# Optimization experiments

Measured on AMD Instinct MI355X. Metric: run time of the kernel, lower is better.

The kernel has to match this reference:

```python
import jax, jax.numpy as jnp
import numpy as np

N = 100000   # nodes
P = 3        # metapaths
E = 800000   # edges per metapath (avg degree 8)
IN = 128     # in_size
H = 4        # layer_num_heads
D = 32       # out_size per head
HID = 64     # semantic attention hidden
NEG_SLOPE = 0.2


def setup_inputs() -> dict:
    key = jax.random.key(0)
    ks = jax.random.split(key, 10)
    h = jax.random.normal(ks[0], (N, IN), jnp.float32)
    edge_src = jax.random.randint(ks[1], (P, E), 0, N, dtype=jnp.int32).astype(jnp.int64)
    edge_dst = jax.random.randint(ks[2], (P, E), 0, N, dtype=jnp.int32).astype(jnp.int64)
    W = jax.random.normal(ks[3], (P, IN, H * D), jnp.float32) * 0.05
    attn_l = jax.random.normal(ks[4], (P, H, D), jnp.float32) * 0.05
    attn_r = jax.random.normal(ks[5], (P, H, D), jnp.float32) * 0.05
    bias = jnp.zeros((P, H * D), jnp.float32)
    sa_w1 = jax.random.normal(ks[6], (H * D, HID), jnp.float32) * 0.05
    sa_b1 = jnp.zeros((HID,), jnp.float32)
    sa_w2 = jax.random.normal(ks[7], (HID, 1), jnp.float32) * 0.05
    return {"h": h, "edge_src": edge_src, "edge_dst": edge_dst, "W": W,
            "attn_l": attn_l, "attn_r": attn_r, "bias": bias,
            "sa_w1": sa_w1, "sa_b1": sa_b1, "sa_w2": sa_w2}


def _gat_conv(h, src, dst, Wp, al, ar, bp):
    # DGL GATConv: project, per-edge additive attention, edge softmax over dst, scatter-sum.
    n = h.shape[0]
    feat = (h @ Wp).reshape(n, H, D)              # [N,H,D]
    el = (feat * al).sum(-1)                      # [N,H]
    er = (feat * ar).sum(-1)                      # [N,H]
    e = jax.nn.leaky_relu(el[src] + er[dst], NEG_SLOPE)   # [E,H]
    emax = jax.ops.segment_max(e, dst, num_segments=n)    # [N,H]
    emax = jnp.where(jnp.isfinite(emax), emax, 0.0)       # zero-in-degree guard
    ex = jnp.exp(e - emax[dst])                            # [E,H]
    denom = jax.ops.segment_sum(ex, dst, num_segments=n)   # [N,H]
    alpha = ex / jnp.maximum(denom[dst], 1e-9)              # [E,H]
    msg = alpha[:, :, None] * feat[src]                     # [E,H,D]
    out = jax.ops.segment_sum(msg, dst, num_segments=n)     # [N,H,D]
    return out.reshape(n, H * D) + bp


def reference(h, edge_src, edge_dst, W, attn_l, attn_r, bias, sa_w1, sa_b1, sa_w2):
    embs = []
    for p in range(P):  # small fixed metapath set
        embs.append(_gat_conv(h, edge_src[p], edge_dst[p], W[p], attn_l[p], attn_r[p], bias[p]))
    z = jnp.stack(embs, axis=1)                 # [N,P,H*D]
    # SemanticAttention: MLP score, mean over nodes, softmax over metapaths
    w = (jnp.tanh(z @ sa_w1 + sa_b1) @ sa_w2).mean(0)   # [P,1]
    beta = jax.nn.softmax(w, axis=0)                     # [P,1]
    return (beta[None, :, :] * z).sum(1)                 # [N,H*D]
```

## Files before the change

kernel.cpp:

```cpp
#include <hip/hip_runtime.h>
#include <hip/hip_bf16.h>
#include <math.h>

#define NN 100000
#define NP 3
#define NE 800000
#define NH 4
#define ND 32
#define HD 128
#define NHID 64

#define SLW 256
#define SBK 512
#define GB 391
#define NBLK 196
#define ECHUNK 4096
#define EPT 16
#define EMAX 2368

typedef __attribute__((ext_vector_type(8))) short short8;
typedef __attribute__((ext_vector_type(4))) float f32x4;

__device__ __forceinline__ unsigned short f2bf(float f) {
  union { float f; unsigned int u; } v; v.f = f;
  unsigned int r = v.u + 0x7FFFu + ((v.u >> 16) & 1u);
  return (unsigned short)(r >> 16);
}
__device__ __forceinline__ float bf2f(unsigned short u) {
  return __uint_as_float(((unsigned int)u) << 16);
}
__device__ __forceinline__ float tanh_fast(float x) {
  return 1.f - 2.f / (1.f + __expf(2.f * x));
}

__global__ __launch_bounds__(256) void prep_fill_kernel(
    const float* __restrict__ h, const float* __restrict__ W, const float* __restrict__ W1,
    const int* __restrict__ src_all, const int* __restrict__ dst_all,
    unsigned short* __restrict__ hb, unsigned short* __restrict__ WT,
    unsigned short* __restrict__ W1T, float* __restrict__ s,
    int* __restrict__ cntA, int* __restrict__ baseA, int* __restrict__ pairs) {
  __shared__ int hist[SBK];
  __shared__ int scanb[SBK];
  const int tid = threadIdx.x;
  const int bx = blockIdx.x;
  if (bx < 12500) {
    int i = bx * 256 + tid;
    if (i < NN * 32) {
      float4 v = ((const float4*)h)[i];
      ushort4 o;
      o.x = f2bf(v.x); o.y = f2bf(v.y); o.z = f2bf(v.z); o.w = f2bf(v.w);
      ((ushort4*)hb)[i] = o;
    }
    if (i < NP * 128 * 128) {
      int p = i >> 14, r = i & 16383, n = r >> 7, k = r & 127;
      WT[i] = f2bf(W[(size_t)p * 16384 + k * 128 + n]);
    }
    if (i < NHID * 128) {
      int n = i >> 7, k = i & 127;
      W1T[i] = f2bf(W1[(size_t)k * NHID + n]);
    }
    if (i < 4) s[i] = 0.f;
    return;
  }
  const int b2 = bx - 12500;
  const int p = b2 / NBLK, blk = b2 % NBLK;
  const int* dstp = dst_all + (size_t)p * NE;
  const int* srcp = src_all + (size_t)p * NE;
  hist[tid] = 0; hist[tid + 256] = 0;
  __syncthreads();
  int dv[EPT], sv[EPT];
#pragma unroll
  for (int k = 0; k < EPT; ++k) {
    int e = blk * ECHUNK + k * 256 + tid;
    dv[k] = -1; sv[k] = 0;
    if (e < NE) {
      dv[k] = __builtin_nontemporal_load(dstp + e);
      sv[k] = __builtin_nontemporal_load(srcp + e);
    }
    if (dv[k] >= 0) atomicAdd(&hist[(unsigned)dv[k] >> 8], 1);
  }
  __syncthreads();
  scanb[tid] = hist[tid]; scanb[tid + 256] = hist[tid + 256];
  __syncthreads();
  for (int off = 1; off < SBK; off <<= 1) {
    int a0 = (tid >= off) ? scanb[tid - off] : 0;
    int a1 = scanb[tid + 256 - off];
    __syncthreads();
    scanb[tid] += a0; scanb[tid + 256] += a1;
    __syncthreads();
  }
  int c0 = hist[tid], c1 = hist[tid + 256];
  int b0 = scanb[tid] - c0, b1 = scanb[tid + 256] - c1;
  int* cA = cntA + ((size_t)p * NBLK + blk) * SBK;
  int* bA = baseA + ((size_t)p * NBLK + blk) * SBK;
  cA[tid] = c0; cA[tid + 256] = c1;
  bA[tid] = b0; bA[tid + 256] = b1;
  __syncthreads();
  scanb[tid] = b0; scanb[tid + 256] = b1;
  hist[tid] = 0; hist[tid + 256] = 0;
  __syncthreads();
  int* prp = pairs + (size_t)p * NE + (size_t)blk * ECHUNK;
#pragma unroll
  for (int k = 0; k < EPT; ++k) {
    if (dv[k] >= 0) {
      int sl = (unsigned)dv[k] >> 8;
      int pos = scanb[sl] + atomicAdd(&hist[sl], 1);
      prp[pos] = ((dv[k] & 255) << 17) | sv[k];
    }
  }
}

__global__ __launch_bounds__(256) void gemm_mfma_kernel(
    const unsigned short* __restrict__ hb, const unsigned short* __restrict__ WT_all,
    const float* __restrict__ al_all, const float* __restrict__ ar_all,
    unsigned short* __restrict__ featb_all, float* __restrict__ el_all,
    float* __restrict__ er_all) {
  __shared__ unsigned short Bs[128 * 128];
  const int p = blockIdx.y;
  const unsigned short* WTp = WT_all + (size_t)p * 16384;
#pragma unroll
  for (int it = 0; it < 8; ++it)
    ((float4*)Bs)[it * 256 + threadIdx.x] = ((const float4*)WTp)[it * 256 + threadIdx.x];
  __syncthreads();

  const int wid = threadIdx.x >> 6, lane = threadIdx.x & 63;
  const int c = lane & 15, q = lane >> 4;
  const int tile = blockIdx.x * 4 + wid;
  const int tc = tile < 6250 ? tile : 6249;

  f32x4 acc[8];
#pragma unroll
  for (int t = 0; t < 8; ++t) acc[t] = (f32x4){0.f, 0.f, 0.f, 0.f};

  const unsigned short* arow = hb + (size_t)(tc * 16 + c) * 128 + q * 8;
#pragma unroll
  for (int kc = 0; kc < 4; ++kc) {
    short8 a = *(const short8*)(arow + kc * 32);
#pragma unroll
    for (int t = 0; t < 8; ++t) {
      short8 b = *(const short8*)(Bs + (size_t)(t * 16 + c) * 128 + kc * 32 + q * 8);
      acc[t] = __builtin_amdgcn_mfma_f32_16x16x32_bf16(a, b, acc[t], 0, 0, 0);
    }
  }
  if (tile >= 6250) return;

  unsigned short* featb = featb_all + (size_t)p * NN * 128;
#pragma unroll
  for (int t = 0; t < 8; ++t)
#pragma unroll
    for (int i = 0; i < 4; ++i)
      featb[(size_t)(tc * 16 + q * 4 + i) * 128 + t * 16 + c] = f2bf(acc[t][i]);

  const float* al = al_all + p * 128;
  const float* ar = ar_all + p * 128;
  float alv[8], arv[8];
#pragma unroll
  for (int t = 0; t < 8; ++t) { alv[t] = al[t * 16 + c]; arv[t] = ar[t * 16 + c]; }
  float elp[4][4], erp[4][4];
#pragma unroll
  for (int i = 0; i < 4; ++i)
#pragma unroll
    for (int hh = 0; hh < 4; ++hh) {
      elp[i][hh] = acc[2 * hh][i] * alv[2 * hh] + acc[2 * hh + 1][i] * alv[2 * hh + 1];
      erp[i][hh] = acc[2 * hh][i] * arv[2 * hh] + acc[2 * hh + 1][i] * arv[2 * hh + 1];
    }
#pragma unroll
  for (int m = 1; m <= 8; m <<= 1)
#pragma unroll
    for (int i = 0; i < 4; ++i)
#pragma unroll
      for (int hh = 0; hh < 4; ++hh) {
        elp[i][hh] += __shfl_xor(elp[i][hh], m);
        erp[i][hh] += __shfl_xor(erp[i][hh], m);
      }
  if (c == 0) {
    float* el = el_all + (size_t)p * NN * 4;
    float* er = er_all + (size_t)p * NN * 4;
#pragma unroll
    for (int i = 0; i < 4; ++i) {
      int row = tc * 16 + q * 4 + i;
      *(float4*)(el + (size_t)row * 4) = make_float4(elp[i][0], elp[i][1], elp[i][2], elp[i][3]);
      *(float4*)(er + (size_t)row * 4) = make_float4(erp[i][0], erp[i][1], erp[i][2], erp[i][3]);
    }
  }
}

__global__ __launch_bounds__(512) void fillB2a_kernel(
    const int* __restrict__ cntA, const int* __restrict__ baseA,
    const int* __restrict__ pairs, int* __restrict__ srtpk,
    int2* __restrict__ rowidx, int* __restrict__ btot) {
  __shared__ int scnt[NBLK];
  __shared__ int sbase[NBLK];
  __shared__ int scum[NBLK];
  __shared__ int totE;
  __shared__ int hist[SLW];
  __shared__ int start[SLW];
  __shared__ int wcur[SLW];
  __shared__ int earr[EMAX];
  const int tid = threadIdx.x;
  const int p = blockIdx.y, sl = blockIdx.x;
  const size_t base = ((size_t)p * GB + sl) * EMAX;

  for (int b = tid; b < NBLK; b += 512) {
    scnt[b] = cntA[((size_t)p * NBLK + b) * SBK + sl];
    sbase[b] = baseA[((size_t)p * NBLK + b) * SBK + sl];
  }
  if (tid < SLW) hist[tid] = 0;
  __syncthreads();
  if (tid < NBLK) scum[tid] = scnt[tid];
  __syncthreads();
  for (int off = 1; off < NBLK; off <<= 1) {
    int a = (tid < NBLK && tid >= off) ? scum[tid - off] : 0;
    __syncthreads();
    if (tid < NBLK) scum[tid] += a;
    __syncthreads();
  }
  if (tid == NBLK - 1) { int t = scum[NBLK - 1]; totE = t > EMAX ? EMAX : t; }
  int excl = (tid < NBLK) ? scum[tid] - scnt[tid] : 0;
  __syncthreads();
  if (tid < NBLK) scum[tid] = excl;
  __syncthreads();
  const int total = totE;
  const int* prp = pairs + (size_t)p * NE;
  for (int e = tid; e < total; e += 512) {
    int lo = 0, hi = NBLK - 1;
    while (lo < hi) { int mid = (lo + hi + 1) >> 1; if (scum[mid] <= e) lo = mid; else hi = mid - 1; }
    int pk = prp[(size_t)lo * ECHUNK + sbase[lo] + (e - scum[lo])];
    earr[e] = pk;
    atomicAdd(&hist[pk >> 17], 1);
  }
  __syncthreads();
  if (tid < SLW) start[tid] = hist[tid];
  __syncthreads();
  for (int off = 1; off < SLW; off <<= 1) {
    int a = (tid < SLW && tid >= off) ? start[tid - off] : 0;
    __syncthreads();
    if (tid < SLW) start[tid] += a;
    __syncthreads();
  }
  if (tid < SLW) { int st = start[tid] - hist[tid]; start[tid] = st; wcur[tid] = st; }
  __syncthreads();
  for (int e = tid; e < total; e += 512) {
    int pk = earr[e];
    int pos = atomicAdd(&wcur[pk >> 17], 1);
    srtpk[base + pos] = pk;
  }
  if (tid < SLW) {
    int n = sl * SLW + tid;
    if (n < NN) rowidx[(size_t)p * NN + n] = make_int2((int)(base + start[tid]), hist[tid]);
  }
  if (tid == 0) btot[p * GB + sl] = total;
}

__global__ __launch_bounds__(256) void fillB2b_kernel(
    const int* __restrict__ srtpk, const int* __restrict__ btot,
    const float* __restrict__ el_all, const float* __restrict__ er_all,
    float4* __restrict__ xs) {
  const int p = blockIdx.y, sl = blockIdx.x;
  const int total = btot[p * GB + sl];
  const size_t base = ((size_t)p * GB + sl) * EMAX;
  const float* el = el_all + (size_t)p * NN * 4;
  const float* er = er_all + (size_t)p * NN * 4;
  for (int i = threadIdx.x; i < total; i += 256) {
    int pk = srtpk[base + i];
    int src = pk & 0x1FFFF, dl = pk >> 17;
    int n = sl * SLW + dl;
    float4 ev = *(const float4*)(el + (size_t)src * 4);
    float4 rv = *(const float4*)(er + (size_t)n * 4);
    float4 x;
    float e0 = ev.x + rv.x; e0 = fmaxf(e0, 0.2f * e0); x.x = __expf(e0);
    float e1 = ev.y + rv.y; e1 = fmaxf(e1, 0.2f * e1); x.y = __expf(e1);
    float e2 = ev.z + rv.z; e2 = fmaxf(e2, 0.2f * e2); x.z = __expf(e2);
    float e3 = ev.w + rv.w; e3 = fmaxf(e3, 0.2f * e3); x.w = __expf(e3);
    xs[base + i] = x;
  }
}

__global__ __launch_bounds__(256) void gather4_kernel(
    const unsigned short* __restrict__ featb_all, const int* __restrict__ srtpk,
    const float* __restrict__ xs, const int2* __restrict__ rowidx,
    const float* __restrict__ bias_all, unsigned short* __restrict__ zb) {
  const int p = blockIdx.y;
  const unsigned short* featb = featb_all + (size_t)p * NN * 128;
  const int q = threadIdx.x >> 4;
  const int c16 = threadIdx.x & 15;
  const int hh = c16 >> 2;
  const int n = blockIdx.x * 16 + q;
  int2 rd = rowidx[(size_t)p * NN + n];
  const int rbase = rd.x, deg = rd.y;

  float acc[8] = {0.f, 0.f, 0.f, 0.f, 0.f, 0.f, 0.f, 0.f};
  float dsum = 0.f;

  for (int j = 0; j < deg; j += 4) {
#pragma unroll
    for (int u = 0; u < 4; ++u) {
      int jj = j + u;
      bool v = jj < deg;
      int idx = rbase + jj;
      int pk = v ? srtpk[idx] : 0;
      float x = v ? xs[(size_t)idx * 4 + hh] : 0.f;
      int s = pk & 0x1FFFF;
      short8 f = *(const short8*)(featb + (size_t)s * 128 + c16 * 8);
      dsum += x;
#pragma unroll
      for (int k = 0; k < 8; ++k) acc[k] += x * bf2f((unsigned short)f[k]);
    }
  }

  float rdn = dsum > 0.f ? 1.f / dsum : 0.f;
  const float* bias = bias_all + p * 128 + c16 * 8;
  float4 b0 = *(const float4*)(bias);
  float4 b1 = *(const float4*)(bias + 4);
  short8 o;
  o[0] = f2bf(acc[0] * rdn + b0.x); o[1] = f2bf(acc[1] * rdn + b0.y);
  o[2] = f2bf(acc[2] * rdn + b0.z); o[3] = f2bf(acc[3] * rdn + b0.w);
  o[4] = f2bf(acc[4] * rdn + b1.x); o[5] = f2bf(acc[5] * rdn + b1.y);
  o[6] = f2bf(acc[6] * rdn + b1.z); o[7] = f2bf(acc[7] * rdn + b1.w);
  *(short8*)(zb + (size_t)n * (NP * 128) + p * 128 + c16 * 8) = o;
}

__global__ __launch_bounds__(256) void sem_mfma_kernel(
    const unsigned short* __restrict__ zb, const unsigned short* __restrict__ W1T,
    const float* __restrict__ b1, const float* __restrict__ w2,
    float* __restrict__ s) {
  __shared__ float red3[3];
  if (threadIdx.x < 3) red3[threadIdx.x] = 0.f;
  __syncthreads();
  const int wid = threadIdx.x >> 6, lane = threadIdx.x & 63;
  const int tile = blockIdx.x * 4 + wid;
  const bool active = tile < 18750;
  const int tc = active ? tile : 18749;
  const int c = lane & 15, q = lane >> 4;
  f32x4 acc[4];
#pragma unroll
  for (int t = 0; t < 4; ++t) acc[t] = (f32x4){0.f, 0.f, 0.f, 0.f};

  const unsigned short* arow = zb + (size_t)(tc * 16 + c) * 128 + q * 8;
  const unsigned short* brow = W1T + (size_t)c * 128 + q * 8;
#pragma unroll
  for (int kc = 0; kc < 4; ++kc) {
    short8 a = *(const short8*)(arow + kc * 32);
#pragma unroll
    for (int t = 0; t < 4; ++t) {
      short8 b = *(const short8*)(brow + (size_t)t * 16 * 128 + kc * 32);
      acc[t] = __builtin_amdgcn_mfma_f32_16x16x32_bf16(a, b, acc[t], 0, 0, 0);
    }
  }
  float part[4] = {0.f, 0.f, 0.f, 0.f};
#pragma unroll
  for (int t = 0; t < 4; ++t) {
    float bb = b1[t * 16 + c], ww = w2[t * 16 + c];
#pragma unroll
    for (int i = 0; i < 4; ++i) part[i] += tanh_fast(acc[t][i] + bb) * ww;
  }
#pragma unroll
  for (int m = 1; m <= 8; m <<= 1)
#pragma unroll
    for (int i = 0; i < 4; ++i) part[i] += __shfl_xor(part[i], m);
  if (active && c == 0) {
#pragma unroll
    for (int i = 0; i < 4; ++i)
      atomicAdd(&red3[(tc * 16 + q * 4 + i) % 3], part[i]);
  }
  __syncthreads();
  if (threadIdx.x < 3) atomicAdd(&s[threadIdx.x], red3[threadIdx.x]);
}

__global__ __launch_bounds__(256) void final_kernel(
    const unsigned short* __restrict__ zb, const float* __restrict__ s,
    float* __restrict__ out) {
  int i = blockIdx.x * blockDim.x + threadIdx.x;
  if (i >= NN * 16) return;
  float w0 = s[0] * (1.f / NN), w1 = s[1] * (1.f / NN), w2c = s[2] * (1.f / NN);
  float m = fmaxf(w0, fmaxf(w1, w2c));
  float e0 = __expf(w0 - m), e1 = __expf(w1 - m), e2 = __expf(w2c - m);
  float inv = 1.f / (e0 + e1 + e2);
  float b0 = e0 * inv, b1 = e1 * inv, b2 = e2 * inv;
  int n = i >> 4, g = i & 15;
  const unsigned short* zr = zb + (size_t)n * (NP * 128) + g * 8;
  ushort4 u0a = *(const ushort4*)(zr);
  ushort4 u0b = *(const ushort4*)(zr + 4);
  ushort4 u1a = *(const ushort4*)(zr + 128);
  ushort4 u1b = *(const ushort4*)(zr + 132);
  ushort4 u2a = *(const ushort4*)(zr + 256);
  ushort4 u2b = *(const ushort4*)(zr + 260);
  float4 oa, ob;
  oa.x = b0 * bf2f(u0a.x) + b1 * bf2f(u1a.x) + b2 * bf2f(u2a.x);
  oa.y = b0 * bf2f(u0a.y) + b1 * bf2f(u1a.y) + b2 * bf2f(u2a.y);
  oa.z = b0 * bf2f(u0a.z) + b1 * bf2f(u1a.z) + b2 * bf2f(u2a.z);
  oa.w = b0 * bf2f(u0a.w) + b1 * bf2f(u1a.w) + b2 * bf2f(u2a.w);
  ob.x = b0 * bf2f(u0b.x) + b1 * bf2f(u1b.x) + b2 * bf2f(u2b.x);
  ob.y = b0 * bf2f(u0b.y) + b1 * bf2f(u1b.y) + b2 * bf2f(u2b.y);
  ob.z = b0 * bf2f(u0b.z) + b1 * bf2f(u1b.z) + b2 * bf2f(u2b.z);
  ob.w = b0 * bf2f(u0b.w) + b1 * bf2f(u1b.w) + b2 * bf2f(u2b.w);
  float* op = out + (size_t)n * 128 + g * 8;
  *(float4*)op = oa;
  *(float4*)(op + 4) = ob;
}

extern "C" void kernel_launch(void* const* d_in, const int* in_sizes, int n_in,
                              void* d_out, int out_size, void* d_ws, size_t ws_size,
                              hipStream_t stream) {
  const float* h    = (const float*)d_in[0];
  const int*   esrc = (const int*)d_in[1];
  const int*   edst = (const int*)d_in[2];
  const float* W    = (const float*)d_in[3];
  const float* al   = (const float*)d_in[4];
  const float* ar   = (const float*)d_in[5];
  const float* bias = (const float*)d_in[6];
  const float* w1   = (const float*)d_in[7];
  const float* b1   = (const float*)d_in[8];
  const float* w2   = (const float*)d_in[9];
  float* out = (float*)d_out;

  unsigned short* zb    = (unsigned short*)d_ws;
  unsigned short* featb = zb + (size_t)38400000;
  unsigned short* WT    = featb + (size_t)38400000;
  unsigned short* W1T   = WT + 49152;
  float* el   = (float*)(W1T + 8192);
  float* er   = el + (size_t)1200000;
  float* s    = er + (size_t)1200000;
  int2* rowidx = (int2*)(s + 16);
  int* btot  = (int*)(rowidx + (size_t)NP * NN);
  int* srtpk = btot + 1280;
  int* cntA  = srtpk + (size_t)NP * GB * EMAX;
  int* baseA = cntA + (size_t)NP * NBLK * SBK;
  int* pairs = baseA + (size_t)NP * NBLK * SBK;
  unsigned short* hb = (unsigned short*)(pairs + (size_t)NP * NE);
  float* xs = (float*)cntA;

  prep_fill_kernel<<<12500 + NP * NBLK, 256, 0, stream>>>(
      h, W, w1, esrc, edst, hb, WT, W1T, s, cntA, baseA, pairs);

  dim3 bGrid(GB, NP);
  fillB2a_kernel<<<bGrid, 512, 0, stream>>>(cntA, baseA, pairs, srtpk, rowidx, btot);

  dim3 gemmGrid(NN / 64 + 1, NP);
  gemm_mfma_kernel<<<gemmGrid, 256, 0, stream>>>(hb, WT, al, ar, featb, el, er);

  fillB2b_kernel<<<bGrid, 256, 0, stream>>>(srtpk, btot, el, er, (float4*)xs);

  dim3 gatherGrid(NN / 16, NP);
  gather4_kernel<<<gatherGrid, 256, 0, stream>>>(featb, srtpk, xs, rowidx, bias, zb);

  sem_mfma_kernel<<<(18750 + 3) / 4, 256, 0, stream>>>(zb, W1T, b1, w2, s);
  final_kernel<<<(NN * 16 + 255) / 256, 256, 0, stream>>>(zb, s, out);
}
```

Before: 446.3 us.

## Fuse h bf16 conversion into GEMM, loop metapaths, compute edge weights in gather

The separate pass that converts h to bf16 is removed. The GEMM now loads fp32 rows of h once, converts them in registers, and reuses them across all three metapaths, reloading each metapath's weights into LDS inside the block. The fillB2b kernel that precomputed per-edge exp weights is gone: the gather computes leaky-relu and exp inline from el[src] and er[dst], which removes one kernel and the xs write and read traffic. In exchange, each edge's exp is recomputed by all 16 lanes of its row group, and the GEMM's parallelism across metapaths is now serialized within each block.

```diff
diff --git a/kernel.cpp b/kernel.cpp
--- a/kernel.cpp
+++ b/kernel.cpp
@@ -17,6 +17,7 @@
 #define ECHUNK 4096
 #define EPT 16
 #define EMAX 2368
+#define PREPB 224
 
 typedef __attribute__((ext_vector_type(8))) short short8;
 typedef __attribute__((ext_vector_type(4))) float f32x4;
@@ -34,35 +35,29 @@
 }
 
 __global__ __launch_bounds__(256) void prep_fill_kernel(
-    const float* __restrict__ h, const float* __restrict__ W, const float* __restrict__ W1,
+    const float* __restrict__ W, const float* __restrict__ W1,
     const int* __restrict__ src_all, const int* __restrict__ dst_all,
-    unsigned short* __restrict__ hb, unsigned short* __restrict__ WT,
-    unsigned short* __restrict__ W1T, float* __restrict__ s,
+    unsigned short* __restrict__ WT, unsigned short* __restrict__ W1T,
+    float* __restrict__ s,
     int* __restrict__ cntA, int* __restrict__ baseA, int* __restrict__ pairs) {
   __shared__ int hist[SBK];
   __shared__ int scanb[SBK];
   const int tid = threadIdx.x;
   const int bx = blockIdx.x;
-  if (bx < 12500) {
+  if (bx < PREPB) {
     int i = bx * 256 + tid;
-    if (i < NN * 32) {
-      float4 v = ((const float4*)h)[i];
-      ushort4 o;
-      o.x = f2bf(v.x); o.y = f2bf(v.y); o.z = f2bf(v.z); o.w = f2bf(v.w);
-      ((ushort4*)hb)[i] = o;
-    }
     if (i < NP * 128 * 128) {
       int p = i >> 14, r = i & 16383, n = r >> 7, k = r & 127;
       WT[i] = f2bf(W[(size_t)p * 16384 + k * 128 + n]);
-    }
-    if (i < NHID * 128) {
-      int n = i >> 7, k = i & 127;
-      W1T[i] = f2bf(W1[(size_t)k * NHID + n]);
-    }
-    if (i < 4) s[i] = 0.f;
+    } else {
+      int i2 = i - NP * 128 * 128;
+      int n = i2 >> 7, k = i2 & 127;
+      W1T[i2] = f2bf(W1[(size_t)k * NHID + n]);
+    }
+    if (bx == 0 && tid < 4) s[tid] = 0.f;
     return;
   }
-  const int b2 = bx - 12500;
+  const int b2 = bx - PREPB;
   const int p = b2 / NBLK, blk = b2 % NBLK;
   const int* dstp = dst_all + (size_t)p * NE;
   const int* srcp = src_all + (size_t)p * NE;
@@ -110,77 +105,91 @@
   }
 }
 
-__global__ __launch_bounds__(256) void gemm_mfma_kernel(
-    const unsigned short* __restrict__ hb, const unsigned short* __restrict__ WT_all,
+__global__ __launch_bounds__(256) void gemm2_kernel(
+    const float* __restrict__ h, const unsigned short* __restrict__ WT_all,
     const float* __restrict__ al_all, const float* __restrict__ ar_all,
     unsigned short* __restrict__ featb_all, float* __restrict__ el_all,
     float* __restrict__ er_all) {
   __shared__ unsigned short Bs[128 * 128];
-  const int p = blockIdx.y;
-  const unsigned short* WTp = WT_all + (size_t)p * 16384;
-#pragma unroll
-  for (int it = 0; it < 8; ++it)
-    ((float4*)Bs)[it * 256 + threadIdx.x] = ((const float4*)WTp)[it * 256 + threadIdx.x];
-  __syncthreads();
-
   const int wid = threadIdx.x >> 6, lane = threadIdx.x & 63;
   const int c = lane & 15, q = lane >> 4;
   const int tile = blockIdx.x * 4 + wid;
   const int tc = tile < 6250 ? tile : 6249;
 
-  f32x4 acc[8];
-#pragma unroll
-  for (int t = 0; t < 8; ++t) acc[t] = (f32x4){0.f, 0.f, 0.f, 0.f};
-
-  const unsigned short* arow = hb + (size_t)(tc * 16 + c) * 128 + q * 8;
+  short8 afr[4];
+  const float* hrow = h + (size_t)(tc * 16 + c) * 128 + q * 8;
 #pragma unroll
   for (int kc = 0; kc < 4; ++kc) {
-    short8 a = *(const short8*)(arow + kc * 32);
-#pragma unroll
-    for (int t = 0; t < 8; ++t) {
-      short8 b = *(const short8*)(Bs + (size_t)(t * 16 + c) * 128 + kc * 32 + q * 8);
-      acc[t] = __builtin_amdgcn_mfma_f32_16x16x32_bf16(a, b, acc[t], 0, 0, 0);
-    }
-  }
-  if (tile >= 6250) return;
-
-  unsigned short* featb = featb_all + (size_t)p * NN * 128;
-#pragma unroll
-  for (int t = 0; t < 8; ++t)
+    float4 a0 = *(const float4*)(hrow + kc * 32);
+    float4 a1 = *(const float4*)(hrow + kc * 32 + 4);
+    short8 a;
+    a[0] = (short)f2bf(a0.x); a[1] = (short)f2bf(a0.y);
+    a[2] = (short)f2bf(a0.z); a[3] = (short)f2bf(a0.w);
+    a[4] = (short)f2bf(a1.x); a[5] = (short)f2bf(a1.y);
+    a[6] = (short)f2bf(a1.z); a[7] = (short)f2bf(a1.w);
+    afr[kc] = a;
+  }
+
+  for (int p = 0; p < NP; ++p) {
+    const unsigned short* WTp = WT_all + (size_t)p * 16384;
+    __syncthreads();
+#pragma unroll
+    for (int it = 0; it < 8; ++it)
+      ((float4*)Bs)[it * 256 + threadIdx.x] = ((const float4*)WTp)[it * 256 + threadIdx.x];
+    __syncthreads();
+
+    f32x4 acc[8];
+#pragma unroll
+    for (int t = 0; t < 8; ++t) acc[t] = (f32x4){0.f, 0.f, 0.f, 0.f};
+#pragma unroll
+    for (int kc = 0; kc < 4; ++kc) {
+      short8 a = afr[kc];
+#pragma unroll
+      for (int t = 0; t < 8; ++t) {
+        short8 b = *(const short8*)(Bs + (size_t)(t * 16 + c) * 128 + kc * 32 + q * 8);
+        acc[t] = __builtin_amdgcn_mfma_f32_16x16x32_bf16(a, b, acc[t], 0, 0, 0);
+      }
+    }
+    if (tile >= 6250) continue;
+
+    unsigned short* featb = featb_all + (size_t)p * NN * 128;
+#pragma unroll
+    for (int t = 0; t < 8; ++t)
+#pragma unroll
+      for (int i = 0; i < 4; ++i)
+        featb[(size_t)(tc * 16 + q * 4 + i) * 128 + t * 16 + c] = f2bf(acc[t][i]);
+
+    const float* al = al_all + p * 128;
+    const float* ar = ar_all + p * 128;
+    float alv[8], arv[8];
+#pragma unroll
+    for (int t = 0; t < 8; ++t) { alv[t] = al[t * 16 + c]; arv[t] = ar[t * 16 + c]; }
+    float elp[4][4], erp[4][4];
 #pragma unroll
     for (int i = 0; i < 4; ++i)
-      featb[(size_t)(tc * 16 + q * 4 + i) * 128 + t * 16 + c] = f2bf(acc[t][i]);
-
-  const float* al = al_all + p * 128;
-  const float* ar = ar_all + p * 128;
-  float alv[8], arv[8];
-#pragma unroll
-  for (int t = 0; t < 8; ++t) { alv[t] = al[t * 16 + c]; arv[t] = ar[t * 16 + c]; }
-  float elp[4][4], erp[4][4];
-#pragma unroll
-  for (int i = 0; i < 4; ++i)
-#pragma unroll
-    for (int hh = 0; hh < 4; ++hh) {
-      elp[i][hh] = acc[2 * hh][i] * alv[2 * hh] + acc[2 * hh + 1][i] * alv[2 * hh + 1];
-      erp[i][hh] = acc[2 * hh][i] * arv[2 * hh] + acc[2 * hh + 1][i] * arv[2 * hh + 1];
-    }
-#pragma unroll
-  for (int m = 1; m <= 8; m <<= 1)
-#pragma unroll
-    for (int i = 0; i < 4; ++i)
 #pragma unroll
       for (int hh = 0; hh < 4; ++hh) {
-        elp[i][hh] += __shfl_xor(elp[i][hh], m);
-        erp[i][hh] += __shfl_xor(erp[i][hh], m);
+        elp[i][hh] = acc[2 * hh][i] * alv[2 * hh] + acc[2 * hh + 1][i] * alv[2 * hh + 1];
+        erp[i][hh] = acc[2 * hh][i] * arv[2 * hh] + acc[2 * hh + 1][i] * arv[2 * hh + 1];
       }
-  if (c == 0) {
-    float* el = el_all + (size_t)p * NN * 4;
-    float* er = er_all + (size_t)p * NN * 4;
-#pragma unroll
-    for (int i = 0; i < 4; ++i) {
-      int row = tc * 16 + q * 4 + i;
-      *(float4*)(el + (size_t)row * 4) = make_float4(elp[i][0], elp[i][1], elp[i][2], elp[i][3]);
-      *(float4*)(er + (size_t)row * 4) = make_float4(erp[i][0], erp[i][1], erp[i][2], erp[i][3]);
+#pragma unroll
+    for (int m = 1; m <= 8; m <<= 1)
+#pragma unroll
+      for (int i = 0; i < 4; ++i)
+#pragma unroll
+        for (int hh = 0; hh < 4; ++hh) {
+          elp[i][hh] += __shfl_xor(elp[i][hh], m);
+          erp[i][hh] += __shfl_xor(erp[i][hh], m);
+        }
+    if (c == 0) {
+      float* el = el_all + (size_t)p * NN * 4;
+      float* er = er_all + (size_t)p * NN * 4;
+#pragma unroll
+      for (int i = 0; i < 4; ++i) {
+        int row = tc * 16 + q * 4 + i;
+        *(float4*)(el + (size_t)row * 4) = make_float4(elp[i][0], elp[i][1], elp[i][2], elp[i][3]);
+        *(float4*)(er + (size_t)row * 4) = make_float4(erp[i][0], erp[i][1], erp[i][2], erp[i][3]);
+      }
     }
   }
 }
@@ -252,42 +261,21 @@
   if (tid == 0) btot[p * GB + sl] = total;
 }
 
-__global__ __launch_bounds__(256) void fillB2b_kernel(
-    const int* __restrict__ srtpk, const int* __restrict__ btot,
+__global__ __launch_bounds__(256) void gather5_kernel(
+    const unsigned short* __restrict__ featb_all, const int* __restrict__ srtpk,
     const float* __restrict__ el_all, const float* __restrict__ er_all,
-    float4* __restrict__ xs) {
-  const int p = blockIdx.y, sl = blockIdx.x;
-  const int total = btot[p * GB + sl];
-  const size_t base = ((size_t)p * GB + sl) * EMAX;
-  const float* el = el_all + (size_t)p * NN * 4;
-  const float* er = er_all + (size_t)p * NN * 4;
-  for (int i = threadIdx.x; i < total; i += 256) {
-    int pk = srtpk[base + i];
-    int src = pk & 0x1FFFF, dl = pk >> 17;
-    int n = sl * SLW + dl;
-    float4 ev = *(const float4*)(el + (size_t)src * 4);
-    float4 rv = *(const float4*)(er + (size_t)n * 4);
-    float4 x;
-    float e0 = ev.x + rv.x; e0 = fmaxf(e0, 0.2f * e0); x.x = __expf(e0);
-    float e1 = ev.y + rv.y; e1 = fmaxf(e1, 0.2f * e1); x.y = __expf(e1);
-    float e2 = ev.z + rv.z; e2 = fmaxf(e2, 0.2f * e2); x.z = __expf(e2);
-    float e3 = ev.w + rv.w; e3 = fmaxf(e3, 0.2f * e3); x.w = __expf(e3);
-    xs[base + i] = x;
-  }
-}
-
-__global__ __launch_bounds__(256) void gather4_kernel(
-    const unsigned short* __restrict__ featb_all, const int* __restrict__ srtpk,
-    const float* __restrict__ xs, const int2* __restrict__ rowidx,
-    const float* __restrict__ bias_all, unsigned short* __restrict__ zb) {
+    const int2* __restrict__ rowidx, const float* __restrict__ bias_all,
+    unsigned short* __restrict__ zb) {
   const int p = blockIdx.y;
   const unsigned short* featb = featb_all + (size_t)p * NN * 128;
+  const float* el = el_all + (size_t)p * NN * 4;
   const int q = threadIdx.x >> 4;
   const int c16 = threadIdx.x & 15;
   const int hh = c16 >> 2;
   const int n = blockIdx.x * 16 + q;
   int2 rd = rowidx[(size_t)p * NN + n];
   const int rbase = rd.x, deg = rd.y;
+  const float ern = er_all[((size_t)p * NN + n) * 4 + hh];
 
   float acc[8] = {0.f, 0.f, 0.f, 0.f, 0.f, 0.f, 0.f, 0.f};
   float dsum = 0.f;
@@ -299,8 +287,13 @@
       bool v = jj < deg;
       int idx = rbase + jj;
       int pk = v ? srtpk[idx] : 0;
-      float x = v ? xs[(size_t)idx * 4 + hh] : 0.f;
       int s = pk & 0x1FFFF;
+      float x = 0.f;
+      if (v) {
+        float e = el[(size_t)s * 4 + hh] + ern;
+        e = fmaxf(e, 0.2f * e);
+        x = __expf(e);
+      }
       short8 f = *(const short8*)(featb + (size_t)s * 128 + c16 * 8);
       dsum += x;
 #pragma unroll
@@ -427,22 +420,17 @@
   int* cntA  = srtpk + (size_t)NP * GB * EMAX;
   int* baseA = cntA + (size_t)NP * NBLK * SBK;
   int* pairs = baseA + (size_t)NP * NBLK * SBK;
-  unsigned short* hb = (unsigned short*)(pairs + (size_t)NP * NE);
-  float* xs = (float*)cntA;
-
-  prep_fill_kernel<<<12500 + NP * NBLK, 256, 0, stream>>>(
-      h, W, w1, esrc, edst, hb, WT, W1T, s, cntA, baseA, pairs);
+
+  prep_fill_kernel<<<PREPB + NP * NBLK, 256, 0, stream>>>(
+      W, w1, esrc, edst, WT, W1T, s, cntA, baseA, pairs);
 
   dim3 bGrid(GB, NP);
   fillB2a_kernel<<<bGrid, 512, 0, stream>>>(cntA, baseA, pairs, srtpk, rowidx, btot);
 
-  dim3 gemmGrid(NN / 64 + 1, NP);
-  gemm_mfma_kernel<<<gemmGrid, 256, 0, stream>>>(hb, WT, al, ar, featb, el, er);
-
-  fillB2b_kernel<<<bGrid, 256, 0, stream>>>(srtpk, btot, el, er, (float4*)xs);
+  gemm2_kernel<<<1563, 256, 0, stream>>>(h, WT, al, ar, featb, el, er);
 
   dim3 gatherGrid(NN / 16, NP);
-  gather4_kernel<<<gatherGrid, 256, 0, stream>>>(featb, srtpk, xs, rowidx, bias, zb);
+  gather5_kernel<<<gatherGrid, 256, 0, stream>>>(featb, srtpk, el, er, rowidx, bias, zb);
 
   sem_mfma_kernel<<<(18750 + 3) / 4, 256, 0, stream>>>(zb, W1T, b1, w2, s);
   final_kernel<<<(NN * 16 + 255) / 256, 256, 0, stream>>>(zb, s, out);
```

Result: faster. 436.3 us (-2.2%).
